# Performance work log

Hardware: AMD Instinct MI355X
Metric: run time of the kernel (lower is better)

The kernel has to match this reference:

```python
import jax, jax.numpy as jnp
import numpy as np

KS = 3
PAD = 1
N = KS * KS  # 9 sampling taps


def conv2d(x, w, b=None):
    out = jax.lax.conv_general_dilated(
        x, w, window_strides=(1, 1), padding=((PAD, PAD), (PAD, PAD)),
        dimension_numbers=('NCHW', 'OIHW', 'NCHW'))
    if b is not None:
        out = out + b[None, :, None, None]
    return out


def deform_conv(x, w_p, b_p, w_m, b_m, w_c):
    """Modulated deformable conv (DCNv2, pure-python reference style)."""
    b, c, h, w = x.shape
    offset = conv2d(x, w_p, b_p)               # [b, 2N, h, w]
    m = jax.nn.sigmoid(conv2d(x, w_m, b_m))    # [b, N, h, w]
    xp = jnp.pad(x, ((0, 0), (0, 0), (PAD, PAD), (PAD, PAD)))
    hp, wp = h + 2 * PAD, w + 2 * PAD
    # kernel-relative offsets p_n and base grid p_0 (coords in padded image)
    r = jnp.arange(-(KS - 1) // 2, (KS - 1) // 2 + 1, dtype=x.dtype)
    pn_x, pn_y = jnp.meshgrid(r, r, indexing='ij')
    pn = jnp.concatenate([pn_x.reshape(-1), pn_y.reshape(-1)])  # [2N]
    p0_x, p0_y = jnp.meshgrid(jnp.arange(1, h + 1, dtype=x.dtype),
                              jnp.arange(1, w + 1, dtype=x.dtype), indexing='ij')
    p0 = jnp.concatenate([jnp.tile(p0_x[None], (N, 1, 1)),
                          jnp.tile(p0_y[None], (N, 1, 1))])     # [2N, h, w]
    p = jnp.transpose(offset + p0[None] + pn[None, :, None, None], (0, 2, 3, 1))  # [b,h,w,2N]
    px, py = p[..., :N], p[..., N:]
    fx, fy = jnp.floor(px), jnp.floor(py)
    q_lt_x = jnp.clip(fx, 0, hp - 1)
    q_lt_y = jnp.clip(fy, 0, wp - 1)
    q_rb_x = jnp.clip(fx + 1, 0, hp - 1)
    q_rb_y = jnp.clip(fy + 1, 0, wp - 1)
    px = jnp.clip(px, 0, hp - 1)
    py = jnp.clip(py, 0, wp - 1)
    # bilinear weights for the 4 integer corners
    g_lt = (1 + (q_lt_x - px)) * (1 + (q_lt_y - py))
    g_rb = (1 - (q_rb_x - px)) * (1 - (q_rb_y - py))
    g_lb = (1 + (q_lt_x - px)) * (1 - (q_rb_y - py))
    g_rt = (1 - (q_rb_x - px)) * (1 + (q_lt_y - py))
    xf = xp.reshape(b, c, hp * wp)

    def gather(qx, qy):
        idx = (qx * wp + qy).astype(jnp.int32).reshape(b, 1, h * w * N)
        idx = jnp.broadcast_to(idx, (b, c, h * w * N))
        return jnp.take_along_axis(xf, idx, axis=2).reshape(b, c, h, w, N)

    x_off = (g_lt[:, None] * gather(q_lt_x, q_lt_y)
             + g_rb[:, None] * gather(q_rb_x, q_rb_y)
             + g_lb[:, None] * gather(q_lt_x, q_rb_y)
             + g_rt[:, None] * gather(q_rb_x, q_lt_y))   # [b,c,h,w,N]
    x_off = x_off * jnp.transpose(m, (0, 2, 3, 1))[:, None]  # modulation
    # Conv2d(kernel=ks, stride=ks) over the reshaped taps == einsum over (c, n)
    return jnp.einsum('bchwn,ocn->bohw', x_off, w_c.reshape(w_c.shape[0], c, N))


def setup_inputs() -> dict:
    key = jax.random.key(0)
    ks = jax.random.split(key, 12)
    b, dim, hid, H, W = 8, 256, 1024, 28, 28
    inp = {
        'x': jax.random.normal(ks[0], (b, dim, H, W), jnp.float32),
        'w_p1': jax.random.normal(ks[1], (2 * N, dim, KS, KS), jnp.float32) * 0.01,
        'b_p1': jnp.zeros((2 * N,), jnp.float32),
        'w_m1': jax.random.normal(ks[2], (N, dim, KS, KS), jnp.float32) * 0.05,
        'b_m1': jnp.zeros((N,), jnp.float32),
        'w_c1': jax.random.normal(ks[3], (hid, dim, KS, KS), jnp.float32) * 0.02,
        'w_p2': jax.random.normal(ks[4], (2 * N, hid, KS, KS), jnp.float32) * 0.01,
        'b_p2': jnp.zeros((2 * N,), jnp.float32),
        'w_m2': jax.random.normal(ks[5], (N, hid, KS, KS), jnp.float32) * 0.05,
        'b_m2': jnp.zeros((N,), jnp.float32),
        'w_c2': jax.random.normal(ks[6], (dim, hid, KS, KS), jnp.float32) * 0.01,
    }
    return inp


def reference(x, w_p1, b_p1, w_m1, b_m1, w_c1, w_p2, b_p2, w_m2, b_m2, w_c2):
    h = jax.nn.relu(deform_conv(x, w_p1, b_p1, w_m1, b_m1, w_c1))
    # dropout p=0.0 -> identity (eval)
    return deform_conv(h, w_p2, b_p2, w_m2, b_m2, w_c2)
```

## Files before the change

### kernel.cpp

```cpp
#include <hip/hip_runtime.h>
#include <hip/hip_bf16.h>
#include <math.h>

#define B 8
#define HH 28
#define WDIM 28
#define PIX 784
#define PPIX 900
#define M_TOT 6272
#define NK 9
#define C1 256
#define HID 1024
#define OUT2 256
#define K1 (C1*9)
#define NY 2560
#define KSP1 12

typedef short short8_t __attribute__((ext_vector_type(8)));
typedef unsigned short us8 __attribute__((ext_vector_type(8)));
typedef unsigned short us4 __attribute__((ext_vector_type(4)));
typedef float f32x4 __attribute__((ext_vector_type(4)));

__device__ inline float bf2f(unsigned short u){ union{unsigned i; float f;} w; w.i=((unsigned)u)<<16; return w.f; }
__device__ inline unsigned short f2bf(float f){ union{float ff; unsigned i;} w; w.ff=f; unsigned u=w.i; return (unsigned short)((u + 0x7FFFu + ((u>>16)&1u))>>16); }

__device__ inline void gload16(const void* g, void* l) {
  __builtin_amdgcn_global_load_lds((const __attribute__((address_space(1))) void*)g,
                                   (__attribute__((address_space(3))) void*)l, 16, 0, 0);
}

__device__ inline int xcd_swz(int bid, int nwg) {
  int q = nwg >> 3, r = nwg & 7;
  int xcd = bid & 7, idx = bid >> 3;
  int base = (xcd < r) ? xcd * (q + 1) : r * (q + 1) + (xcd - r) * q;
  return base + idx;
}

__global__ __launch_bounds__(256) void ring_zero(unsigned short* __restrict__ buf, int C)
{
  int r = blockIdx.x % 116, b = blockIdx.x / 116;
  int h, w;
  if (r < 30)      { h = 0;  w = r; }
  else if (r < 60) { h = 29; w = r - 30; }
  else if (r < 88) { h = r - 59; w = 0; }
  else             { h = r - 87; w = 29; }
  unsigned short* row = buf + ((size_t)b * PPIX + h * 30 + w) * C;
  for (int c = threadIdx.x * 8; c < C; c += 2048)
    *(us8*)(row + c) = us8{0,0,0,0,0,0,0,0};
}

__global__ __launch_bounds__(256) void xpose_kernel(
    const float* __restrict__ x, unsigned short* __restrict__ xclp, int C)
{
  __shared__ unsigned short tile[32][33];
  int b = blockIdx.z, c0 = blockIdx.y * 32, p0 = blockIdx.x * 32;
  int tx = threadIdx.x & 31, ty = threadIdx.x >> 5;
  for (int i = ty; i < 32; i += 8) {
    int c = c0 + i, p = p0 + tx;
    unsigned short v = 0;
    if (p < PIX) v = f2bf(x[((size_t)b * C + c) * PIX + p]);
    tile[i][tx] = v;
  }
  __syncthreads();
  for (int i = ty; i < 32; i += 8) {
    int p = p0 + i, c = c0 + tx;
    if (p < PIX) {
      int h = p / WDIM, w = p % WDIM;
      xclp[((size_t)b * PPIX + (h + 1) * 30 + (w + 1)) * C + c] = tile[tx][i];
    }
  }
}

__global__ __launch_bounds__(256) void wrep_kernel(
    const float* __restrict__ w, unsigned short* __restrict__ wr)
{
  __shared__ float lds[K1];
  int o = blockIdx.x;
  for (int i = threadIdx.x; i < K1; i += 256) lds[i] = w[(size_t)o * K1 + i];
  __syncthreads();
  for (int k = threadIdx.x; k < K1; k += 256) {
    int n = k >> 8, c = k & 255;
    wr[(size_t)o * K1 + k] = f2bf(lds[c * 9 + n]);
  }
}

__global__ __launch_bounds__(256) void wprep_kernel(
    const float* __restrict__ wp, const float* __restrict__ wm,
    unsigned short* __restrict__ wpr)
{
  __shared__ float lds[K1];
  int ch = blockIdx.x;
  const float* src = nullptr;
  if (ch < 18) src = wp + (size_t)ch * K1;
  else if (ch < 27) src = wm + (size_t)(ch - 18) * K1;
  for (int i = threadIdx.x; i < K1; i += 256) lds[i] = src ? src[i] : 0.f;
  __syncthreads();
  for (int k = threadIdx.x; k < K1; k += 256) {
    int n = k >> 8, c = k & 255;
    wpr[(size_t)ch * K1 + k] = f2bf(lds[c * 9 + n]);
  }
}

__global__ __launch_bounds__(256) void wy2prep_kernel(
    const float* __restrict__ wc2, const float* __restrict__ wp2,
    const float* __restrict__ wm2, unsigned short* __restrict__ wy)
{
  __shared__ float lds[HID * 9];
  int bid = blockIdx.x;
  if (bid >= 283) {
    int j = 2547 + (bid - 283);
    for (int c = threadIdx.x; c < HID; c += 256) wy[(size_t)j * HID + c] = 0;
    return;
  }
  const float* src;
  if (bid < 256) src = wc2 + (size_t)bid * HID * 9;
  else {
    int ch = bid - 256;
    src = (ch < 18) ? wp2 + (size_t)ch * HID * 9 : wm2 + (size_t)(ch - 18) * HID * 9;
  }
  for (int i = threadIdx.x; i < HID * 9; i += 256) lds[i] = src[i];
  __syncthreads();
  #pragma unroll
  for (int n = 0; n < 9; ++n) {
    int j = (bid < 256) ? n * 256 + bid : 2304 + n * 27 + (bid - 256);
    for (int c = threadIdx.x; c < HID; c += 256)
      wy[(size_t)j * HID + c] = f2bf(lds[c * 9 + n]);
  }
}

template<int C, int KSPLIT>
__global__ __launch_bounds__(256) void pconv_mfma(
    const unsigned short* __restrict__ xclp,
    const unsigned short* __restrict__ wpr,
    float* __restrict__ pmpart)
{
  __shared__ unsigned short As[2][128 * 64];
  __shared__ unsigned short Ws[2][32 * 64];
  const int K = 9 * C;
  int t = threadIdx.x, lane = t & 63, wv = t >> 6;
  int m0 = blockIdx.x * 128;
  int kz = blockIdx.y;
  int wm = (wv & 1) * 64, wo = (wv >> 1) * 16;
  f32x4 acc[4];
  #pragma unroll
  for (int i = 0; i < 4; ++i) acc[i] = {0.f, 0.f, 0.f, 0.f};
  long pbase[4];
  #pragma unroll
  for (int i = 0; i < 4; ++i) {
    int L = i * 256 + t, row = L >> 3;
    int m = m0 + row, b = m / PIX, pix = m - b * PIX;
    int h = pix / WDIM, w = pix - h * WDIM;
    pbase[i] = ((long)b * PPIX + (h + 1) * 30 + (w + 1)) * C;
  }
  auto stage = [&](int buf, int kk) {
    int n = kk / C, c0 = kk - n * C;
    long doff = (long)(((n / 3) - 1) * 30 + (n % 3) - 1) * C + c0;
    #pragma unroll
    for (int i = 0; i < 4; ++i) {
      int L = i * 256 + t, row = L >> 3, ch = L & 7;
      const char* src = (const char*)(xclp + pbase[i] + doff) + ((ch ^ (row & 7)) << 4);
      gload16(src, (char*)As[buf] + (size_t)(i * 256 + (wv << 6)) * 16);
    }
    {
      int row = t >> 3, ch = t & 7;
      const char* src = (const char*)(wpr + (size_t)row * K + kk) + ((ch ^ (row & 7)) << 4);
      gload16(src, (char*)Ws[buf] + (size_t)(wv << 6) * 16);
    }
  };

  int kbeg = kz * (K / KSPLIT), kend = kbeg + K / KSPLIT;
  stage(0, kbeg);
  asm volatile("s_waitcnt vmcnt(0)" ::: "memory");
  __syncthreads();
  int cur = 0;
  for (int k0 = kbeg; k0 < kend; k0 += 64, cur ^= 1) {
    if (k0 + 64 < kend) stage(cur ^ 1, k0 + 64);
    #pragma unroll
    for (int ks = 0; ks < 2; ++ks) {
      short8_t af[4], bq;
      {
        int row = wo + (lane & 15), ch = ks * 4 + (lane >> 4);
        bq = *(const short8_t*)((const char*)Ws[cur] + row * 128 + ((ch ^ (row & 7)) << 4));
      }
      #pragma unroll
      for (int fm = 0; fm < 4; ++fm) {
        int row = wm + fm * 16 + (lane & 15), ch = ks * 4 + (lane >> 4);
        af[fm] = *(const short8_t*)((const char*)As[cur] + row * 128 + ((ch ^ (row & 7)) << 4));
      }
      #pragma unroll
      for (int fm = 0; fm < 4; ++fm)
        acc[fm] = __builtin_amdgcn_mfma_f32_16x16x32_bf16(af[fm], bq, acc[fm], 0, 0, 0);
    }
    asm volatile("s_waitcnt vmcnt(0)" ::: "memory");
    __syncthreads();
  }
  float* dst = pmpart + (size_t)kz * M_TOT * 32;
  #pragma unroll
  for (int fm = 0; fm < 4; ++fm)
    #pragma unroll
    for (int r = 0; r < 4; ++r) {
      int ml = m0 + wm + fm * 16 + (lane >> 4) * 4 + r;
      int o = wo + (lane & 15);
      dst[(size_t)ml * 32 + o] = acc[fm][r];
    }
}

__device__ inline void mktab_emit(int i, int m, int n, float ox, float oy, float om,
                                  const float* b_p, const float* b_m,
                                  int4* tabOff, float4* tabG)
{
  int bidx = m / PIX, pix = m % PIX;
  int hh = pix / WDIM, ww = pix % WDIM;
  float px = ox + b_p[n]     + (float)(hh + 1) + (float)(n / 3 - 1);
  float py = oy + b_p[9 + n] + (float)(ww + 1) + (float)(n % 3 - 1);
  float msk = 1.f / (1.f + expf(-(om + b_m[n])));
  float fx = floorf(px), fy = floorf(py);
  float qlx = fminf(fmaxf(fx, 0.f), 29.f);
  float qly = fminf(fmaxf(fy, 0.f), 29.f);
  float qrx = fminf(fmaxf(fx + 1.f, 0.f), 29.f);
  float qry = fminf(fmaxf(fy + 1.f, 0.f), 29.f);
  float pxc = fminf(fmaxf(px, 0.f), 29.f);
  float pyc = fminf(fmaxf(py, 0.f), 29.f);
  float glt = (1.f + (qlx - pxc)) * (1.f + (qly - pyc));
  float grb = (1.f - (qrx - pxc)) * (1.f - (qry - pyc));
  float glb = (1.f + (qlx - pxc)) * (1.f - (qry - pyc));
  float grt = (1.f - (qrx - pxc)) * (1.f + (qly - pyc));
  int ax = (int)qlx, ay = (int)qly, bx = (int)qrx, by = (int)qry;
  int pb = bidx * PPIX;
  tabOff[i] = make_int4(pb + ax * 30 + ay, pb + bx * 30 + by,
                        pb + ax * 30 + by, pb + bx * 30 + ay);
  tabG[i]   = make_float4(glt * msk, grb * msk, glb * msk, grt * msk);
}

template<int KSPLIT>
__global__ __launch_bounds__(256) void mktab_kernel(
    const float* __restrict__ pmpart,
    const float* __restrict__ b_p, const float* __restrict__ b_m,
    int4* __restrict__ tabOff, float4* __restrict__ tabG)
{
  int i = blockIdx.x * 256 + threadIdx.x;
  if (i >= M_TOT * NK) return;
  int m = i / NK, n = i % NK;
  float ox = 0.f, oy = 0.f, om = 0.f;
  #pragma unroll
  for (int kz = 0; kz < KSPLIT; ++kz) {
    const float* q = pmpart + (size_t)kz * M_TOT * 32 + (size_t)m * 32;
    ox += q[n]; oy += q[9 + n]; om += q[18 + n];
  }
  mktab_emit(i, m, n, ox, oy, om, b_p, b_m, tabOff, tabG);
}

__global__ __launch_bounds__(256) void mktab2_kernel(
    const unsigned short* __restrict__ Y,
    const float* __restrict__ b_p, const float* __restrict__ b_m,
    int4* __restrict__ tabOff, float4* __restrict__ tabG)
{
  int i = blockIdx.x * 256 + threadIdx.x;
  if (i >= M_TOT * NK) return;
  int m = i / NK, n = i % NK;
  int b = m / PIX, pix = m % PIX;
  int h = pix / WDIM, w = pix % WDIM;
  int q0 = b * PPIX + (h + 1) * 30 + (w + 1);
  float ox = 0.f, oy = 0.f, om = 0.f;
  #pragma unroll
  for (int tap = 0; tap < NK; ++tap) {
    int q = q0 + (tap / 3 - 1) * 30 + (tap % 3 - 1);
    const unsigned short* base = Y + (size_t)q * NY + 2304 + tap * 27;
    ox += bf2f(base[n]); oy += bf2f(base[9 + n]); om += bf2f(base[18 + n]);
  }
  mktab_emit(i, m, n, ox, oy, om, b_p, b_m, tabOff, tabG);
}

template<int CIN>
__global__ __launch_bounds__(256) void sample_cl_kernel(
    const unsigned short* __restrict__ xclp,
    const int4* __restrict__ tabO, const float4* __restrict__ tabG,
    unsigned short* __restrict__ A)
{
  constexpr int LPM = CIN / 8;
  constexpr int MPB = 256 / LPM;
  int mi = threadIdx.x / LPM;
  int c0 = (threadIdx.x % LPM) * 8;
  int m = blockIdx.x * MPB + mi;
  const int4*  to = tabO + (size_t)m * NK;
  const float4* tg = tabG + (size_t)m * NK;
  unsigned short* Arow = A + (size_t)m * (NK * CIN);
  #pragma unroll
  for (int n = 0; n < NK; ++n) {
    int4 o = to[n]; float4 g = tg[n];
    us8 a0 = *(const us8*)(xclp + (size_t)o.x * CIN + c0);
    us8 a1 = *(const us8*)(xclp + (size_t)o.y * CIN + c0);
    us8 a2 = *(const us8*)(xclp + (size_t)o.z * CIN + c0);
    us8 a3 = *(const us8*)(xclp + (size_t)o.w * CIN + c0);
    us8 r;
    #pragma unroll
    for (int j = 0; j < 8; ++j) {
      float v = g.x * bf2f(a0[j]) + g.y * bf2f(a1[j])
              + g.z * bf2f(a2[j]) + g.w * bf2f(a3[j]);
      r[j] = f2bf(v);
    }
    *(us8*)(Arow + n * CIN + c0) = r;
  }
}

template<int TN, int VAR>
__global__ __launch_bounds__(256) void gemm_mfma(
    const unsigned short* __restrict__ A,
    const unsigned short* __restrict__ Wr,
    void* __restrict__ outv,
    int K, int O, int nOt, int nwg)
{
  __shared__ unsigned short As[2][128 * 64];
  __shared__ unsigned short Ws[2][TN * 64];
  constexpr int NFO = TN / 32;
  int t = threadIdx.x, lane = t & 63, wv = t >> 6;
  int swz = xcd_swz(blockIdx.x, nwg);
  int m0 = (swz / nOt) * 128, o0 = (swz % nOt) * TN;
  int wm = (wv & 1) * 64, wo = (wv >> 1) * (TN / 2);
  f32x4 acc[4][NFO];
  #pragma unroll
  for (int i = 0; i < 4; ++i)
    #pragma unroll
    for (int j = 0; j < NFO; ++j)
      acc[i][j] = {0.f, 0.f, 0.f, 0.f};

  auto stage = [&](int buf, int kk) {
    #pragma unroll
    for (int i = 0; i < 4; ++i) {
      int L = i * 256 + t, row = L >> 3, ch = L & 7;
      const char* src = (const char*)(A + (size_t)(m0 + row) * K + kk) + ((ch ^ (row & 7)) << 4);
      gload16(src, (char*)As[buf] + (size_t)(i * 256 + (wv << 6)) * 16);
    }
    #pragma unroll
    for (int i = 0; i < TN / 32; ++i) {
      int L = i * 256 + t, row = L >> 3, ch = L & 7;
      const char* src = (const char*)(Wr + (size_t)(o0 + row) * K + kk) + ((ch ^ (row & 7)) << 4);
      gload16(src, (char*)Ws[buf] + (size_t)(i * 256 + (wv << 6)) * 16);
    }
  };

  stage(0, 0);
  asm volatile("s_waitcnt vmcnt(0)" ::: "memory");
  __syncthreads();
  int cur = 0;
  for (int k0 = 0; k0 < K; k0 += 64, cur ^= 1) {
    if (k0 + 64 < K) stage(cur ^ 1, k0 + 64);
    #pragma unroll
    for (int ks = 0; ks < 2; ++ks) {
      short8_t af[4], bq[NFO];
      #pragma unroll
      for (int fm = 0; fm < 4; ++fm) {
        int row = wm + fm * 16 + (lane & 15), ch = ks * 4 + (lane >> 4);
        af[fm] = *(const short8_t*)((const char*)As[cur] + row * 128 + ((ch ^ (row & 7)) << 4));
      }
      #pragma unroll
      for (int fo = 0; fo < NFO; ++fo) {
        int row = wo + fo * 16 + (lane & 15), ch = ks * 4 + (lane >> 4);
        bq[fo] = *(const short8_t*)((const char*)Ws[cur] + row * 128 + ((ch ^ (row & 7)) << 4));
      }
      #pragma unroll
      for (int fm = 0; fm < 4; ++fm)
        #pragma unroll
        for (int fo = 0; fo < NFO; ++fo)
          acc[fm][fo] = __builtin_amdgcn_mfma_f32_16x16x32_bf16(af[fm], bq[fo], acc[fm][fo], 0, 0, 0);
    }
    asm volatile("s_waitcnt vmcnt(0)" ::: "memory");
    __syncthreads();
  }

  unsigned short* outp = (unsigned short*)outv;
  #pragma unroll
  for (int fm = 0; fm < 4; ++fm)
    #pragma unroll
    for (int r = 0; r < 4; ++r) {
      int m = m0 + wm + fm * 16 + (lane >> 4) * 4 + r;
      size_t base;
      if (VAR == 0) base = (size_t)m * O;
      else {
        int b = m / PIX, pix = m - b * PIX;
        int h = pix / WDIM, w = pix - h * WDIM;
        base = ((size_t)b * PPIX + (h + 1) * 30 + (w + 1)) * (size_t)O;
      }
      #pragma unroll
      for (int fo = 0; fo < NFO; ++fo) {
        int o = o0 + wo + fo * 16 + (lane & 15);
        float v = acc[fm][fo][r];
        if (VAR == 0) v = fmaxf(v, 0.f);
        outp[base + o] = f2bf(v);
      }
    }
}

__global__ __launch_bounds__(256) void depi2_kernel(
    const unsigned short* __restrict__ Y,
    const int4* __restrict__ tabO, const float4* __restrict__ tabG,
    float* __restrict__ out)
{
  __shared__ float tile[256][4];
  int m0 = blockIdx.x * 4;
  int b = m0 / PIX, pix0 = m0 % PIX;
  int g = threadIdx.x >> 6, lane = threadIdx.x & 63;
  int m = m0 + g;
  const int4*  to = tabO + (size_t)m * NK;
  const float4* tg = tabG + (size_t)m * NK;
  f32x4 acc = {0.f, 0.f, 0.f, 0.f};
  #pragma unroll
  for (int n = 0; n < NK; ++n) {
    int4 o4 = to[n]; float4 g4 = tg[n];
    int col = n * 256 + lane * 4;
    us4 y0 = *(const us4*)(Y + (size_t)o4.x * NY + col);
    us4 y1 = *(const us4*)(Y + (size_t)o4.y * NY + col);
    us4 y2 = *(const us4*)(Y + (size_t)o4.z * NY + col);
    us4 y3 = *(const us4*)(Y + (size_t)o4.w * NY + col);
    #pragma unroll
    for (int j = 0; j < 4; ++j)
      acc[j] += g4.x * bf2f(y0[j]) + g4.y * bf2f(y1[j])
              + g4.z * bf2f(y2[j]) + g4.w * bf2f(y3[j]);
  }
  #pragma unroll
  for (int j = 0; j < 4; ++j) tile[lane * 4 + j][g] = acc[j];
  __syncthreads();
  int o = threadIdx.x;
  float4 v = *(const float4*)&tile[o][0];
  *(float4*)&out[((size_t)b * OUT2 + o) * PIX + pix0] = v;
}

extern "C" void kernel_launch(void* const* d_in, const int* in_sizes, int n_in,
                              void* d_out, int out_size, void* d_ws, size_t ws_size,
                              hipStream_t stream)
{
  const float* x    = (const float*)d_in[0];
  const float* w_p1 = (const float*)d_in[1];
  const float* b_p1 = (const float*)d_in[2];
  const float* w_m1 = (const float*)d_in[3];
  const float* b_m1 = (const float*)d_in[4];
  const float* w_c1 = (const float*)d_in[5];
  const float* w_p2 = (const float*)d_in[6];
  const float* b_p2 = (const float*)d_in[7];
  const float* w_m2 = (const float*)d_in[8];
  const float* b_m2 = (const float*)d_in[9];
  const float* w_c2 = (const float*)d_in[10];
  float* out = (float*)d_out;

  char* ws = (char*)d_ws;
  auto align_up = [](size_t v) { return (v + 255) & ~(size_t)255; };
  size_t off = 0;
  unsigned short* xclp = (unsigned short*)(ws + off); off += align_up((size_t)B * PPIX * C1 * 2);
  unsigned short* hcl  = (unsigned short*)(ws + off); off += align_up((size_t)M_TOT * HID * 2);
  unsigned short* Y    = (unsigned short*)(ws + off); off += align_up((size_t)B * PPIX * NY * 2);
  float* pmpart = (float*)(ws + off); off += align_up((size_t)KSP1 * M_TOT * 32 * 4);
  int4*   tabO = (int4*)(ws + off);   off += align_up((size_t)M_TOT * NK * 16);
  float4* tabG = (float4*)(ws + off); off += align_up((size_t)M_TOT * NK * 16);
  unsigned short* wr1  = (unsigned short*)(ws + off); off += align_up((size_t)HID * K1 * 2);
  unsigned short* wy2  = (unsigned short*)(ws + off); off += align_up((size_t)NY * HID * 2);
  unsigned short* wpr1 = (unsigned short*)(ws + off); off += align_up((size_t)32 * K1 * 2);
  unsigned short* Abuf = (unsigned short*)(ws + off); off += align_up((size_t)M_TOT * K1 * 2);

  ring_zero<<<B * 116, 256, 0, stream>>>(xclp, C1);
  ring_zero<<<B * 116, 256, 0, stream>>>(Y, NY);

  xpose_kernel<<<dim3(25, C1 / 32, B), 256, 0, stream>>>(x, xclp, C1);
  wrep_kernel<<<HID, 256, 0, stream>>>(w_c1, wr1);
  wprep_kernel<<<32, 256, 0, stream>>>(w_p1, w_m1, wpr1);
  wy2prep_kernel<<<296, 256, 0, stream>>>(w_c2, w_p2, w_m2, wy2);

  pconv_mfma<C1, KSP1><<<dim3(M_TOT / 128, KSP1), 256, 0, stream>>>(xclp, wpr1, pmpart);
  mktab_kernel<KSP1><<<(M_TOT * NK + 255) / 256, 256, 0, stream>>>(pmpart, b_p1, b_m1, tabO, tabG);
  sample_cl_kernel<C1><<<M_TOT / 8, 256, 0, stream>>>(xclp, tabO, tabG, Abuf);
  {
    int nwg = (M_TOT / 128) * (HID / 128);
    gemm_mfma<128, 0><<<nwg, 256, 0, stream>>>(Abuf, wr1, hcl, K1, HID, HID / 128, nwg);
  }

  {
    int nwg = (M_TOT / 128) * (NY / 128);
    gemm_mfma<128, 3><<<nwg, 256, 0, stream>>>(hcl, wy2, Y, HID, NY, NY / 128, nwg);
  }
  mktab2_kernel<<<(M_TOT * NK + 255) / 256, 256, 0, stream>>>(Y, b_p2, b_m2, tabO, tabG);
  depi2_kernel<<<M_TOT / 4, 256, 0, stream>>>(Y, tabO, tabG, out);
}
```

Baseline: 145.5 us.

## Fuse offset-table builds into sampling kernels and merge prep launches

```diff
diff --git a/kernel.cpp b/kernel.cpp
--- a/kernel.cpp
+++ b/kernel.cpp
@@ -36,9 +36,14 @@
   return base + idx;
 }
 
-__global__ __launch_bounds__(256) void ring_zero(unsigned short* __restrict__ buf, int C)
-{
-  int r = blockIdx.x % 116, b = blockIdx.x / 116;
+__global__ __launch_bounds__(256) void ring_zero2(
+    unsigned short* __restrict__ xclp, unsigned short* __restrict__ Y)
+{
+  int bid = blockIdx.x;
+  unsigned short* buf; int C;
+  if (bid < B * 116) { buf = xclp; C = C1; }
+  else               { buf = Y; C = NY; bid -= B * 116; }
+  int r = bid % 116, b = bid / 116;
   int h, w;
   if (r < 30)      { h = 0;  w = r; }
   else if (r < 60) { h = 29; w = r - 30; }
@@ -71,45 +76,41 @@
   }
 }
 
-__global__ __launch_bounds__(256) void wrep_kernel(
-    const float* __restrict__ w, unsigned short* __restrict__ wr)
-{
-  __shared__ float lds[K1];
-  int o = blockIdx.x;
-  for (int i = threadIdx.x; i < K1; i += 256) lds[i] = w[(size_t)o * K1 + i];
-  __syncthreads();
-  for (int k = threadIdx.x; k < K1; k += 256) {
-    int n = k >> 8, c = k & 255;
-    wr[(size_t)o * K1 + k] = f2bf(lds[c * 9 + n]);
-  }
-}
-
-__global__ __launch_bounds__(256) void wprep_kernel(
-    const float* __restrict__ wp, const float* __restrict__ wm,
-    unsigned short* __restrict__ wpr)
-{
-  __shared__ float lds[K1];
-  int ch = blockIdx.x;
-  const float* src = nullptr;
-  if (ch < 18) src = wp + (size_t)ch * K1;
-  else if (ch < 27) src = wm + (size_t)(ch - 18) * K1;
-  for (int i = threadIdx.x; i < K1; i += 256) lds[i] = src ? src[i] : 0.f;
-  __syncthreads();
-  for (int k = threadIdx.x; k < K1; k += 256) {
-    int n = k >> 8, c = k & 255;
-    wpr[(size_t)ch * K1 + k] = f2bf(lds[c * 9 + n]);
-  }
-}
-
-__global__ __launch_bounds__(256) void wy2prep_kernel(
-    const float* __restrict__ wc2, const float* __restrict__ wp2,
-    const float* __restrict__ wm2, unsigned short* __restrict__ wy)
+__global__ __launch_bounds__(256) void wprep_all(
+    const float* __restrict__ wc1, const float* __restrict__ wp1,
+    const float* __restrict__ wm1, const float* __restrict__ wc2,
+    const float* __restrict__ wp2, const float* __restrict__ wm2,
+    unsigned short* __restrict__ wr1, unsigned short* __restrict__ wpr1,
+    unsigned short* __restrict__ wy2)
 {
   __shared__ float lds[HID * 9];
   int bid = blockIdx.x;
+  if (bid < HID) {
+    for (int i = threadIdx.x; i < K1; i += 256) lds[i] = wc1[(size_t)bid * K1 + i];
+    __syncthreads();
+    for (int k = threadIdx.x; k < K1; k += 256) {
+      int n = k >> 8, c = k & 255;
+      wr1[(size_t)bid * K1 + k] = f2bf(lds[c * 9 + n]);
+    }
+    return;
+  }
+  if (bid < HID + 32) {
+    int ch = bid - HID;
+    const float* src = nullptr;
+    if (ch < 18) src = wp1 + (size_t)ch * K1;
+    else if (ch < 27) src = wm1 + (size_t)(ch - 18) * K1;
+    for (int i = threadIdx.x; i < K1; i += 256) lds[i] = src ? src[i] : 0.f;
+    __syncthreads();
+    for (int k = threadIdx.x; k < K1; k += 256) {
+      int n = k >> 8, c = k & 255;
+      wpr1[(size_t)ch * K1 + k] = f2bf(lds[c * 9 + n]);
+    }
+    return;
+  }
+  bid -= HID + 32;
   if (bid >= 283) {
     int j = 2547 + (bid - 283);
-    for (int c = threadIdx.x; c < HID; c += 256) wy[(size_t)j * HID + c] = 0;
+    for (int c = threadIdx.x; c < HID; c += 256) wy2[(size_t)j * HID + c] = 0;
     return;
   }
   const float* src;
@@ -124,7 +125,7 @@
   for (int n = 0; n < 9; ++n) {
     int j = (bid < 256) ? n * 256 + bid : 2304 + n * 27 + (bid - 256);
     for (int c = threadIdx.x; c < HID; c += 256)
-      wy[(size_t)j * HID + c] = f2bf(lds[c * 9 + n]);
+      wy2[(size_t)j * HID + c] = f2bf(lds[c * 9 + n]);
   }
 }
 
@@ -205,7 +206,7 @@
     }
 }
 
-__device__ inline void mktab_emit(int i, int m, int n, float ox, float oy, float om,
+__device__ inline void mktab_emit(int m, int n, float ox, float oy, float om,
                                   const float* b_p, const float* b_m,
                                   int4* tabOff, float4* tabG)
 {
@@ -227,67 +228,44 @@
   float grt = (1.f - (qrx - pxc)) * (1.f + (qly - pyc));
   int ax = (int)qlx, ay = (int)qly, bx = (int)qrx, by = (int)qry;
   int pb = bidx * PPIX;
-  tabOff[i] = make_int4(pb + ax * 30 + ay, pb + bx * 30 + by,
-                        pb + ax * 30 + by, pb + bx * 30 + ay);
-  tabG[i]   = make_float4(glt * msk, grb * msk, glb * msk, grt * msk);
-}
-
-template<int KSPLIT>
-__global__ __launch_bounds__(256) void mktab_kernel(
+  *tabOff = make_int4(pb + ax * 30 + ay, pb + bx * 30 + by,
+                      pb + ax * 30 + by, pb + bx * 30 + ay);
+  *tabG   = make_float4(glt * msk, grb * msk, glb * msk, grt * msk);
+}
+
+template<int CIN, int KSPLIT>
+__global__ __launch_bounds__(256) void sample_tab_kernel(
+    const unsigned short* __restrict__ xclp,
     const float* __restrict__ pmpart,
     const float* __restrict__ b_p, const float* __restrict__ b_m,
-    int4* __restrict__ tabOff, float4* __restrict__ tabG)
-{
-  int i = blockIdx.x * 256 + threadIdx.x;
-  if (i >= M_TOT * NK) return;
-  int m = i / NK, n = i % NK;
-  float ox = 0.f, oy = 0.f, om = 0.f;
-  #pragma unroll
-  for (int kz = 0; kz < KSPLIT; ++kz) {
-    const float* q = pmpart + (size_t)kz * M_TOT * 32 + (size_t)m * 32;
-    ox += q[n]; oy += q[9 + n]; om += q[18 + n];
-  }
-  mktab_emit(i, m, n, ox, oy, om, b_p, b_m, tabOff, tabG);
-}
-
-__global__ __launch_bounds__(256) void mktab2_kernel(
-    const unsigned short* __restrict__ Y,
-    const float* __restrict__ b_p, const float* __restrict__ b_m,
-    int4* __restrict__ tabOff, float4* __restrict__ tabG)
-{
-  int i = blockIdx.x * 256 + threadIdx.x;
-  if (i >= M_TOT * NK) return;
-  int m = i / NK, n = i % NK;
-  int b = m / PIX, pix = m % PIX;
-  int h = pix / WDIM, w = pix % WDIM;
-  int q0 = b * PPIX + (h + 1) * 30 + (w + 1);
-  float ox = 0.f, oy = 0.f, om = 0.f;
-  #pragma unroll
-  for (int tap = 0; tap < NK; ++tap) {
-    int q = q0 + (tap / 3 - 1) * 30 + (tap % 3 - 1);
-    const unsigned short* base = Y + (size_t)q * NY + 2304 + tap * 27;
-    ox += bf2f(base[n]); oy += bf2f(base[9 + n]); om += bf2f(base[18 + n]);
-  }
-  mktab_emit(i, m, n, ox, oy, om, b_p, b_m, tabOff, tabG);
-}
-
-template<int CIN>
-__global__ __launch_bounds__(256) void sample_cl_kernel(
-    const unsigned short* __restrict__ xclp,
-    const int4* __restrict__ tabO, const float4* __restrict__ tabG,
     unsigned short* __restrict__ A)
 {
   constexpr int LPM = CIN / 8;
   constexpr int MPB = 256 / LPM;
-  int mi = threadIdx.x / LPM;
-  int c0 = (threadIdx.x % LPM) * 8;
-  int m = blockIdx.x * MPB + mi;
-  const int4*  to = tabO + (size_t)m * NK;
-  const float4* tg = tabG + (size_t)m * NK;
-  unsigned short* Arow = A + (size_t)m * (NK * CIN);
+  __shared__ int4   stabO[MPB][NK];
+  __shared__ float4 stabG[MPB][NK];
+  int m0 = blockIdx.x * MPB;
+  int t = threadIdx.x;
+  if (t < MPB * NK) {
+    int ml = t / NK, n = t % NK;
+    int m = m0 + ml;
+    float ox = 0.f, oy = 0.f, om = 0.f;
+    #pragma unroll
+    for (int kz = 0; kz < KSPLIT; ++kz) {
+      const float* q = pmpart + (size_t)kz * M_TOT * 32 + (size_t)m * 32;
+      ox += q[n]; oy += q[9 + n]; om += q[18 + n];
+    }
+    mktab_emit(m, n, ox, oy, om, b_p, b_m, &stabO[ml][n], &stabG[ml][n]);
+  }
+  __syncthreads();
+  int mi = t / LPM;
+  int c0 = (t % LPM) * 8;
+  int m = m0 + mi;
+  (void)m;
+  unsigned short* Arow = A + (size_t)(m0 + mi) * (NK * CIN);
   #pragma unroll
   for (int n = 0; n < NK; ++n) {
-    int4 o = to[n]; float4 g = tg[n];
+    int4 o = stabO[mi][n]; float4 g = stabG[mi][n];
     us8 a0 = *(const us8*)(xclp + (size_t)o.x * CIN + c0);
     us8 a1 = *(const us8*)(xclp + (size_t)o.y * CIN + c0);
     us8 a2 = *(const us8*)(xclp + (size_t)o.z * CIN + c0);
@@ -393,20 +371,36 @@
 
 __global__ __launch_bounds__(256) void depi2_kernel(
     const unsigned short* __restrict__ Y,
-    const int4* __restrict__ tabO, const float4* __restrict__ tabG,
+    const float* __restrict__ b_p, const float* __restrict__ b_m,
     float* __restrict__ out)
 {
+  __shared__ int4   stabO[4][NK];
+  __shared__ float4 stabG[4][NK];
   __shared__ float tile[256][4];
   int m0 = blockIdx.x * 4;
+  int t = threadIdx.x;
+  if (t < 4 * NK) {
+    int g = t / NK, n = t % NK;
+    int m = m0 + g;
+    int b = m / PIX, pix = m % PIX;
+    int h = pix / WDIM, w = pix % WDIM;
+    int q0 = b * PPIX + (h + 1) * 30 + (w + 1);
+    float ox = 0.f, oy = 0.f, om = 0.f;
+    #pragma unroll
+    for (int tap = 0; tap < NK; ++tap) {
+      int q = q0 + (tap / 3 - 1) * 30 + (tap % 3 - 1);
+      const unsigned short* base = Y + (size_t)q * NY + 2304 + tap * 27;
+      ox += bf2f(base[n]); oy += bf2f(base[9 + n]); om += bf2f(base[18 + n]);
+    }
+    mktab_emit(m, n, ox, oy, om, b_p, b_m, &stabO[g][n], &stabG[g][n]);
+  }
+  __syncthreads();
   int b = m0 / PIX, pix0 = m0 % PIX;
-  int g = threadIdx.x >> 6, lane = threadIdx.x & 63;
-  int m = m0 + g;
-  const int4*  to = tabO + (size_t)m * NK;
-  const float4* tg = tabG + (size_t)m * NK;
+  int g = t >> 6, lane = t & 63;
   f32x4 acc = {0.f, 0.f, 0.f, 0.f};
   #pragma unroll
   for (int n = 0; n < NK; ++n) {
-    int4 o4 = to[n]; float4 g4 = tg[n];
+    int4 o4 = stabO[g][n]; float4 g4 = stabG[g][n];
     int col = n * 256 + lane * 4;
     us4 y0 = *(const us4*)(Y + (size_t)o4.x * NY + col);
     us4 y1 = *(const us4*)(Y + (size_t)o4.y * NY + col);
@@ -420,7 +414,7 @@
   #pragma unroll
   for (int j = 0; j < 4; ++j) tile[lane * 4 + j][g] = acc[j];
   __syncthreads();
-  int o = threadIdx.x;
+  int o = t;
   float4 v = *(const float4*)&tile[o][0];
   *(float4*)&out[((size_t)b * OUT2 + o) * PIX + pix0] = v;
 }
@@ -449,24 +443,19 @@
   unsigned short* hcl  = (unsigned short*)(ws + off); off += align_up((size_t)M_TOT * HID * 2);
   unsigned short* Y    = (unsigned short*)(ws + off); off += align_up((size_t)B * PPIX * NY * 2);
   float* pmpart = (float*)(ws + off); off += align_up((size_t)KSP1 * M_TOT * 32 * 4);
-  int4*   tabO = (int4*)(ws + off);   off += align_up((size_t)M_TOT * NK * 16);
-  float4* tabG = (float4*)(ws + off); off += align_up((size_t)M_TOT * NK * 16);
   unsigned short* wr1  = (unsigned short*)(ws + off); off += align_up((size_t)HID * K1 * 2);
   unsigned short* wy2  = (unsigned short*)(ws + off); off += align_up((size_t)NY * HID * 2);
   unsigned short* wpr1 = (unsigned short*)(ws + off); off += align_up((size_t)32 * K1 * 2);
   unsigned short* Abuf = (unsigned short*)(ws + off); off += align_up((size_t)M_TOT * K1 * 2);
 
-  ring_zero<<<B * 116, 256, 0, stream>>>(xclp, C1);
-  ring_zero<<<B * 116, 256, 0, stream>>>(Y, NY);
-
+  ring_zero2<<<2 * B * 116, 256, 0, stream>>>(xclp, Y);
   xpose_kernel<<<dim3(25, C1 / 32, B), 256, 0, stream>>>(x, xclp, C1);
-  wrep_kernel<<<HID, 256, 0, stream>>>(w_c1, wr1);
-  wprep_kernel<<<32, 256, 0, stream>>>(w_p1, w_m1, wpr1);
-  wy2prep_kernel<<<296, 256, 0, stream>>>(w_c2, w_p2, w_m2, wy2);
+  wprep_all<<<HID + 32 + 296, 256, 0, stream>>>(
+      w_c1, w_p1, w_m1, w_c2, w_p2, w_m2, wr1, wpr1, wy2);
 
   pconv_mfma<C1, KSP1><<<dim3(M_TOT / 128, KSP1), 256, 0, stream>>>(xclp, wpr1, pmpart);
-  mktab_kernel<KSP1><<<(M_TOT * NK + 255) / 256, 256, 0, stream>>>(pmpart, b_p1, b_m1, tabO, tabG);
-  sample_cl_kernel<C1><<<M_TOT / 8, 256, 0, stream>>>(xclp, tabO, tabG, Abuf);
+  sample_tab_kernel<C1, KSP1><<<M_TOT / 8, 256, 0, stream>>>(
+      xclp, pmpart, b_p1, b_m1, Abuf);
   {
     int nwg = (M_TOT / 128) * (HID / 128);
     gemm_mfma<128, 0><<<nwg, 256, 0, stream>>>(Abuf, wr1, hcl, K1, HID, HID / 128, nwg);
@@ -476,6 +465,5 @@
     int nwg = (M_TOT / 128) * (NY / 128);
     gemm_mfma<128, 3><<<nwg, 256, 0, stream>>>(hcl, wy2, Y, HID, NY, NY / 128, nwg);
   }
-  mktab2_kernel<<<(M_TOT * NK + 255) / 256, 256, 0, stream>>>(Y, b_p2, b_m2, tabO, tabG);
-  depi2_kernel<<<M_TOT / 4, 256, 0, stream>>>(Y, tabO, tabG, out);
-}
+  depi2_kernel<<<M_TOT / 4, 256, 0, stream>>>(Y, b_p2, b_m2, out);
+}
```

Result: faster. 131.7 us (-9.5%).
